# Performance work log

Measured on AMD Instinct MI355X. Metric: run time of the kernel, lower is better.

Reference implementation:

```python
import jax, jax.numpy as jnp
import numpy as np

STRIDE = 3


def _conv_block(x, W, b):
    # x: (B, L, C) -> windows (B, L-2, 3C) via fixed-stride slicing (faithful to scan_conv)
    B, L, C = x.shape
    Lw = L - STRIDE + 1
    win = jnp.concatenate([x[:, i:Lw + i, :] for i in range(STRIDE)], axis=-1)  # (B, Lw, 3C)
    y = jax.nn.leaky_relu(jnp.einsum('blk,ok->blo', win, W) + b)  # torch Linear: x @ W.T + b
    # zero_gate: zero rows of the *window* tensor zero the output
    mask = (jnp.sum(win, axis=2, keepdims=True) != 0).astype(y.dtype)
    y = y * mask
    # max_pool1d over sequence, kernel=2 stride=2 (floor)
    Lp = y.shape[1] // 2
    y = y[:, :2 * Lp, :].reshape(B, Lp, 2, -1).max(axis=2)
    return y


def setup_inputs() -> dict:
    key = jax.random.key(0)
    ks = jax.random.split(key, 16)
    B, PAD, E, IMG, V = 1024, 30, 512, 2048, 32000
    c1, c2, c3, lin2 = 200, 300, 300, 400
    lin1_in = 2 * c3 + IMG  # flattened (B,2,300) + image -> 600 + 2048
    s = 0.02
    return {
        'image_vectors': jax.random.normal(ks[0], (B, IMG), jnp.float32),
        'sentences': jax.random.randint(ks[1], (B, PAD), 0, V, jnp.int32),
        'embed_table': jax.random.normal(ks[2], (V, E), jnp.float32),
        'W1': jax.random.normal(ks[3], (c1, E * STRIDE), jnp.float32) * s,
        'b1': jnp.zeros((c1,), jnp.float32),
        'W2': jax.random.normal(ks[4], (c2, c1 * STRIDE), jnp.float32) * s,
        'b2': jnp.zeros((c2,), jnp.float32),
        'W3': jax.random.normal(ks[5], (c3, c2 * STRIDE), jnp.float32) * s,
        'b3': jnp.zeros((c3,), jnp.float32),
        'Wm': jax.random.normal(ks[6], (lin2, lin1_in), jnp.float32) * s,
        'bm': jnp.zeros((lin2,), jnp.float32),
        'Wo': jax.random.normal(ks[7], (1, lin2), jnp.float32) * s,
        'bo': jnp.zeros((1,), jnp.float32),
    }


def reference(image_vectors, sentences, embed_table, W1, b1, W2, b2, W3, b3, Wm, bm, Wo, bo):
    x = embed_table[sentences]                       # (B, 30, 512)
    x = _conv_block(x, W1, b1)                       # (B, 14, 200)
    x = _conv_block(x, W2, b2)                       # (B, 6, 300)
    x = _conv_block(x, W3, b3)                       # (B, 2, 300)
    B = x.shape[0]
    feats = jnp.concatenate([x.reshape(B, -1), image_vectors], axis=1)  # (B, 2648)
    h = jax.nn.leaky_relu(feats @ Wm.T + bm)         # (B, 400)
    out = h @ Wo.T + bo                              # (B, 1)
    return out
```

## Files before the change

kernel.cpp:

```cpp
#include <hip/hip_runtime.h>
#include <hip/hip_bf16.h>

#define LEAKY(v) ((v) > 0.0f ? (v) : 0.01f * (v))

constexpr int B_   = 1024;
constexpr int PAD  = 30;
constexpr int E    = 512;
constexpr int IMG  = 2048;
constexpr int C1   = 200;
constexpr int C2   = 300;
constexpr int C3   = 300;
constexpr int LIN2 = 400;

constexpr int NT1P = 16, KT1 = 48;
constexpr int NT2P = 20, KT2 = 21;
constexpr int NT3P = 24, KT3 = 30;
constexpr int NTMP = 28, KTM = 83;
constexpr int FK  = 2656;

constexpr int T1 = NT1P * KT1;
constexpr int T2 = NT2P * KT2;
constexpr int T3 = NT3P * KT3;
constexpr int TM = NTMP * KTM;
constexpr int TTOT = T1 + T2 + T3 + TM;

typedef __attribute__((ext_vector_type(8))) short bf16x8;
typedef __attribute__((ext_vector_type(4))) float f32x4;

__device__ inline unsigned short f2bf(float f) {
    __hip_bfloat16 h = __float2bfloat16(f);
    return *reinterpret_cast<unsigned short*>(&h);
}
__device__ inline float bf2f(unsigned short u) {
    unsigned int b = ((unsigned int)u) << 16;
    return __uint_as_float(b);
}

__global__ __launch_bounds__(256) void convert_all(
    const float* __restrict__ W1, const float* __restrict__ W2,
    const float* __restrict__ W3, const float* __restrict__ Wm,
    unsigned short* __restrict__ W1t, unsigned short* __restrict__ W2t,
    unsigned short* __restrict__ W3t, unsigned short* __restrict__ Wmt)
{
    int idx = blockIdx.x * 256 + threadIdx.x;
    if (idx >= TTOT * 64) return;
    int lane = idx & 63, t = idx >> 6;
    unsigned short v[8];

    if (t < T1) {
        int kk = t % KT1, nt = t / KT1;
        int ch = nt * 16 + (lane & 15);
        int k0 = kk * 32 + (lane >> 4) * 8;
        #pragma unroll
        for (int j = 0; j < 8; ++j)
            v[j] = (ch < C1) ? f2bf(W1[(size_t)ch * (3*E) + k0 + j]) : (unsigned short)0;
        ushort4* dst = reinterpret_cast<ushort4*>(W1t) + (size_t)t * 128 + lane * 2;
        dst[0] = ushort4{v[0],v[1],v[2],v[3]};
        dst[1] = ushort4{v[4],v[5],v[6],v[7]};
    } else if (t < T1 + T2) {
        int tt = t - T1;
        int kk = tt % KT2, nt = tt / KT2;
        int ch = nt * 16 + (lane & 15);
        int rowoff = kk / 7;
        int cbase  = (kk % 7) * 32 + (lane >> 4) * 8;
        #pragma unroll
        for (int j = 0; j < 8; ++j) {
            int c = cbase + j;
            v[j] = (ch < C2 && c < C1) ? f2bf(W2[(size_t)ch * (3*C1) + rowoff * C1 + c])
                                       : (unsigned short)0;
        }
        ushort4* dst = reinterpret_cast<ushort4*>(W2t) + (size_t)tt * 128 + lane * 2;
        dst[0] = ushort4{v[0],v[1],v[2],v[3]};
        dst[1] = ushort4{v[4],v[5],v[6],v[7]};
    } else if (t < T1 + T2 + T3) {
        int tt = t - T1 - T2;
        int kk = tt % KT3, nt = tt / KT3;
        int ch = nt * 16 + (lane & 15);
        int rowoff = kk / 10;
        int cbase  = (kk % 10) * 32 + (lane >> 4) * 8;
        #pragma unroll
        for (int j = 0; j < 8; ++j) {
            int c = cbase + j;
            v[j] = (ch < C3 && c < C2) ? f2bf(W3[(size_t)ch * (3*C2) + rowoff * C2 + c])
                                       : (unsigned short)0;
        }
        ushort4* dst = reinterpret_cast<ushort4*>(W3t) + (size_t)tt * 128 + lane * 2;
        dst[0] = ushort4{v[0],v[1],v[2],v[3]};
        dst[1] = ushort4{v[4],v[5],v[6],v[7]};
    } else {
        int tt = t - T1 - T2 - T3;
        int kk = tt % KTM, nt = tt / KTM;
        int ch = nt * 16 + (lane & 15);
        int kbase = kk * 32 + (lane >> 4) * 8;
        #pragma unroll
        for (int j = 0; j < 8; ++j) {
            int k = kbase + j;
            v[j] = (ch < LIN2 && k < 2648) ? f2bf(Wm[(size_t)ch * 2648 + k])
                                           : (unsigned short)0;
        }
        ushort4* dst = reinterpret_cast<ushort4*>(Wmt) + (size_t)tt * 128 + lane * 2;
        dst[0] = ushort4{v[0],v[1],v[2],v[3]};
        dst[1] = ushort4{v[4],v[5],v[6],v[7]};
    }
}

__global__ __launch_bounds__(512, 4) void conv_fused(
    const int* __restrict__ sent, const float* __restrict__ emb,
    const unsigned short* __restrict__ W1t, const float* __restrict__ b1,
    const unsigned short* __restrict__ W2t, const float* __restrict__ b2,
    const unsigned short* __restrict__ W3t, const float* __restrict__ b3,
    const float* __restrict__ image, unsigned short* __restrict__ feats)
{
    const int blk = blockIdx.x;
    const int tid = threadIdx.x;
    __shared__ unsigned short xs[66 * 512];
    __shared__ float rs[64];
    __shared__ float rs2[36];
    __shared__ float rs3[12];
    char* xsb = reinterpret_cast<char*>(xs);

    const int wid = tid >> 6, lane = tid & 63;
    const int kg = lane >> 4, trow = lane & 15, g = kg;

    for (int r = wid; r < 60; r += 8) {
        int bl = r / 30, rr = r % 30;
        int R = bl * 32 + rr;
        int row = sent[(2 * blk + bl) * PAD + rr];
        const float4* src = reinterpret_cast<const float4*>(emb + (size_t)row * E) + lane * 2;
        float4 e0 = src[0], e1 = src[1];
        float sum = e0.x + e0.y + e0.z + e0.w + e1.x + e1.y + e1.z + e1.w;
        union { ushort4 u4[2]; bf16x8 v; } pk;
        pk.u4[0] = ushort4{f2bf(e0.x), f2bf(e0.y), f2bf(e0.z), f2bf(e0.w)};
        pk.u4[1] = ushort4{f2bf(e1.x), f2bf(e1.y), f2bf(e1.z), f2bf(e1.w)};
        int byteoff = R * 1024 + ((lane ^ (R & 7)) << 4);
        *reinterpret_cast<bf16x8*>(xsb + byteoff) = pk.v;
        for (int off = 32; off; off >>= 1) sum += __shfl_down(sum, off);
        if (lane == 0) rs[R] = sum;
    }
    if (tid < 384) {
        int zi = tid >> 6;
        int R = (zi < 2) ? (30 + zi) : (60 + zi);
        int byteoff = R * 1024 + ((lane ^ (R & 7)) << 4);
        union { ushort4 u4[2]; bf16x8 v; } pk;
        pk.u4[0] = ushort4{0,0,0,0}; pk.u4[1] = ushort4{0,0,0,0};
        *reinterpret_cast<bf16x8*>(xsb + byteoff) = pk.v;
    }
    if (tid < 4) {
        const int pr[4] = {30, 31, 62, 63};
        rs[pr[tid]] = 0.f;
    }
    __syncthreads();

    const bf16x8* wb1 = reinterpret_cast<const bf16x8*>(W1t);
    const bf16x8* wp0 = wb1 + (size_t)((wid    ) * KT1) * 64 + lane;
    const bf16x8* wp1 = wb1 + (size_t)((wid + 8) * KT1) * 64 + lane;

    f32x4 c00={0,0,0,0},c01={0,0,0,0},c02={0,0,0,0},c03={0,0,0,0};
    f32x4 c10={0,0,0,0},c11={0,0,0,0},c12={0,0,0,0},c13={0,0,0,0};

    if (wid < 5) {
        #pragma unroll
        for (int rowoff = 0; rowoff < 3; ++rowoff) {
            const int R0 = trow + rowoff;
            const int R1 = R0 + 16, R2 = R0 + 32, R3 = R0 + 48;
            const int b3_0 = R0 * 1024 + (((R0 & 7) ^ kg) << 4);
            const int b3_1 = R1 * 1024 + (((R1 & 7) ^ kg) << 4);
            const int b3_2 = R2 * 1024 + (((R2 & 7) ^ kg) << 4);
            const int b3_3 = R3 * 1024 + (((R3 & 7) ^ kg) << 4);
            #pragma unroll
            for (int cc = 0; cc < 16; ++cc) {
                const int kk = rowoff * 16 + cc;
                bf16x8 a0 = *reinterpret_cast<const bf16x8*>(xsb + (b3_0 ^ (cc << 6)));
                bf16x8 a1 = *reinterpret_cast<const bf16x8*>(xsb + (b3_1 ^ (cc << 6)));
                bf16x8 a2 = *reinterpret_cast<const bf16x8*>(xsb + (b3_2 ^ (cc << 6)));
                bf16x8 a3 = *reinterpret_cast<const bf16x8*>(xsb + (b3_3 ^ (cc << 6)));
                bf16x8 b0 = wp0[kk * 64];
                bf16x8 b1v = wp1[kk * 64];
                c00 = __builtin_amdgcn_mfma_f32_16x16x32_bf16(a0, b0, c00, 0, 0, 0);
                c01 = __builtin_amdgcn_mfma_f32_16x16x32_bf16(a1, b0, c01, 0, 0, 0);
                c02 = __builtin_amdgcn_mfma_f32_16x16x32_bf16(a2, b0, c02, 0, 0, 0);
                c03 = __builtin_amdgcn_mfma_f32_16x16x32_bf16(a3, b0, c03, 0, 0, 0);
                c10 = __builtin_amdgcn_mfma_f32_16x16x32_bf16(a0, b1v, c10, 0, 0, 0);
                c11 = __builtin_amdgcn_mfma_f32_16x16x32_bf16(a1, b1v, c11, 0, 0, 0);
                c12 = __builtin_amdgcn_mfma_f32_16x16x32_bf16(a2, b1v, c12, 0, 0, 0);
                c13 = __builtin_amdgcn_mfma_f32_16x16x32_bf16(a3, b1v, c13, 0, 0, 0);
            }
        }
    } else {
        #pragma unroll
        for (int rowoff = 0; rowoff < 3; ++rowoff) {
            const int R0 = trow + rowoff;
            const int R1 = R0 + 16, R2 = R0 + 32, R3 = R0 + 48;
            const int b3_0 = R0 * 1024 + (((R0 & 7) ^ kg) << 4);
            const int b3_1 = R1 * 1024 + (((R1 & 7) ^ kg) << 4);
            const int b3_2 = R2 * 1024 + (((R2 & 7) ^ kg) << 4);
            const int b3_3 = R3 * 1024 + (((R3 & 7) ^ kg) << 4);
            #pragma unroll
            for (int cc = 0; cc < 16; ++cc) {
                const int kk = rowoff * 16 + cc;
                bf16x8 a0 = *reinterpret_cast<const bf16x8*>(xsb + (b3_0 ^ (cc << 6)));
                bf16x8 a1 = *reinterpret_cast<const bf16x8*>(xsb + (b3_1 ^ (cc << 6)));
                bf16x8 a2 = *reinterpret_cast<const bf16x8*>(xsb + (b3_2 ^ (cc << 6)));
                bf16x8 a3 = *reinterpret_cast<const bf16x8*>(xsb + (b3_3 ^ (cc << 6)));
                bf16x8 b0 = wp0[kk * 64];
                c00 = __builtin_amdgcn_mfma_f32_16x16x32_bf16(a0, b0, c00, 0, 0, 0);
                c01 = __builtin_amdgcn_mfma_f32_16x16x32_bf16(a1, b0, c01, 0, 0, 0);
                c02 = __builtin_amdgcn_mfma_f32_16x16x32_bf16(a2, b0, c02, 0, 0, 0);
                c03 = __builtin_amdgcn_mfma_f32_16x16x32_bf16(a3, b0, c03, 0, 0, 0);
            }
        }
    }
    __syncthreads();

    for (int idx = tid; idx < 36 * 32; idx += 512) {
        int r = idx >> 5, ck = idx & 31;
        union { ushort4 u4[2]; bf16x8 v; } pk;
        pk.u4[0] = ushort4{0,0,0,0}; pk.u4[1] = ushort4{0,0,0,0};
        *reinterpret_cast<bf16x8*>(xsb + r * 512 + (ck << 4)) = pk.v;
    }
    __syncthreads();

#define EPIM1(MT, CM) do {                                                       \
    int bl = (MT) >> 1;                                                          \
    int mloc = ((MT) & 1) * 16;                                                  \
    _Pragma("unroll")                                                            \
    for (int hf = 0; hf < 2; ++hf) {                                             \
        int wl = mloc + 4 * g + 2 * hf;                                          \
        int tp = wl >> 1;                                                        \
        if (tp < 14) {                                                           \
            float v0 = CM[2*hf] + bia, v1 = CM[2*hf+1] + bia;                    \
            v0 = LEAKY(v0); v1 = LEAKY(v1);                                      \
            int rb = bl * 32 + wl;                                               \
            if (rs[rb] + rs[rb+1] + rs[rb+2] == 0.f) v0 = 0.f;                   \
            if (rs[rb+1] + rs[rb+2] + rs[rb+3] == 0.f) v1 = 0.f;                 \
            int rg = bl * 18 + tp;                                               \
            int bo = rg * 512 + ((((ch) >> 3) ^ (rg & 7)) << 4) + ((ch) & 7) * 2;\
            *reinterpret_cast<unsigned short*>(xsb + bo) = f2bf(fmaxf(v0, v1));  \
        }                                                                        \
    }                                                                            \
} while (0)

#define EPI1(NTI, CA, CB, CC, CD) do {                                           \
    int ch = (wid + 8 * (NTI)) * 16 + trow;                                      \
    if (ch < C1) {                                                               \
        float bia = b1[ch];                                                      \
        EPIM1(0, CA); EPIM1(1, CB); EPIM1(2, CC); EPIM1(3, CD);                  \
    }                                                                            \
} while (0)

    EPI1(0, c00, c01, c02, c03);
    if (wid < 5) {
        EPI1(1, c10, c11, c12, c13);
    }
#undef EPI1
#undef EPIM1
    __syncthreads();

    for (int r = wid; r < 36; r += 8) {
        float s = 0.f;
        #pragma unroll
        for (int j = 0; j < 4; ++j) {
            int e = lane + 64 * j;
            int chunk = e >> 3, within = e & 7;
            s += bf2f(*reinterpret_cast<unsigned short*>(
                xsb + r * 512 + ((chunk ^ (r & 7)) << 4) + within * 2));
        }
        for (int off = 32; off; off >>= 1) s += __shfl_down(s, off);
        if (lane == 0) rs2[r] = s;
    }
    __syncthreads();

    const bf16x8* wb2 = reinterpret_cast<const bf16x8*>(W2t);
    const int nt2a = wid, nt2b = wid + 8;
    const int nt2c = (wid + 16 < NT2P) ? (wid + 16) : (NT2P - 1);
    const bf16x8* q0 = wb2 + (size_t)(nt2a * KT2) * 64 + lane;
    const bf16x8* q1 = wb2 + (size_t)(nt2b * KT2) * 64 + lane;
    const bf16x8* q2 = wb2 + (size_t)(nt2c * KT2) * 64 + lane;

    f32x4 d00={0,0,0,0},d01={0,0,0,0};
    f32x4 d10={0,0,0,0},d11={0,0,0,0};
    f32x4 d20={0,0,0,0},d21={0,0,0,0};

    {
        int kidx = 0;
        #pragma unroll
        for (int rowoff = 0; rowoff < 3; ++rowoff) {
            const int R0 = trow + rowoff;
            const int R1 = R0 + 18;
            const int b3_0 = R0 * 512 + (((R0 & 7) ^ kg) << 4);
            const int b3_1 = R1 * 512 + (((R1 & 7) ^ kg) << 4);
            #pragma unroll
            for (int cc = 0; cc < 7; ++cc, ++kidx) {
                bf16x8 a0 = *reinterpret_cast<const bf16x8*>(xsb + (b3_0 ^ (cc << 6)));
                bf16x8 a1 = *reinterpret_cast<const bf16x8*>(xsb + (b3_1 ^ (cc << 6)));
                bf16x8 b0 = q0[kidx * 64];
                bf16x8 b1v = q1[kidx * 64];
                bf16x8 b2v = q2[kidx * 64];
                d00 = __builtin_amdgcn_mfma_f32_16x16x32_bf16(a0, b0,  d00, 0, 0, 0);
                d01 = __builtin_amdgcn_mfma_f32_16x16x32_bf16(a1, b0,  d01, 0, 0, 0);
                d10 = __builtin_amdgcn_mfma_f32_16x16x32_bf16(a0, b1v, d10, 0, 0, 0);
                d11 = __builtin_amdgcn_mfma_f32_16x16x32_bf16(a1, b1v, d11, 0, 0, 0);
                d20 = __builtin_amdgcn_mfma_f32_16x16x32_bf16(a0, b2v, d20, 0, 0, 0);
                d21 = __builtin_amdgcn_mfma_f32_16x16x32_bf16(a1, b2v, d21, 0, 0, 0);
            }
        }
    }
    __syncthreads();

    for (int idx = tid; idx < 15 * 40; idx += 512) {
        int r = idx / 40, ck = idx % 40;
        union { ushort4 u4[2]; bf16x8 v; } pk;
        pk.u4[0] = ushort4{0,0,0,0}; pk.u4[1] = ushort4{0,0,0,0};
        *reinterpret_cast<bf16x8*>(xsb + r * 640 + (ck << 4)) = pk.v;
    }
    __syncthreads();

#define EPI2F(NT, DA, DB) do {                                                   \
    int ch = (NT) * 16 + trow;                                                   \
    if (ch < C2) {                                                               \
        float bia = b2[ch];                                                      \
        _Pragma("unroll")                                                        \
        for (int hf = 0; hf < 2; ++hf) {                                         \
            int t0 = 4 * g + 2 * hf;                                             \
            if (t0 < 12) {                                                       \
                { float v0 = LEAKY(DA[2*hf]   + bia);                            \
                  float v1 = LEAKY(DA[2*hf+1] + bia);                            \
                  if (rs2[t0] + rs2[t0+1] + rs2[t0+2] == 0.f) v0 = 0.f;          \
                  if (rs2[t0+1] + rs2[t0+2] + rs2[t0+3] == 0.f) v1 = 0.f;        \
                  int rg = (t0 >> 1);                                            \
                  int bo = rg * 640 + ((((ch)>>3) ^ (rg & 7)) << 4) + ((ch)&7)*2;\
                  *reinterpret_cast<unsigned short*>(xsb + bo) = f2bf(fmaxf(v0, v1)); } \
                { float v0 = LEAKY(DB[2*hf]   + bia);                            \
                  float v1 = LEAKY(DB[2*hf+1] + bia);                            \
                  int rb = 18 + t0;                                              \
                  if (rs2[rb] + rs2[rb+1] + rs2[rb+2] == 0.f) v0 = 0.f;          \
                  if (rs2[rb+1] + rs2[rb+2] + rs2[rb+3] == 0.f) v1 = 0.f;        \
                  int rg = 6 + (t0 >> 1);                                        \
                  int bo = rg * 640 + ((((ch)>>3) ^ (rg & 7)) << 4) + ((ch)&7)*2;\
                  *reinterpret_cast<unsigned short*>(xsb + bo) = f2bf(fmaxf(v0, v1)); } \
            }                                                                    \
        }                                                                        \
    }                                                                            \
} while (0)

    EPI2F(nt2a, d00, d01);
    EPI2F(nt2b, d10, d11);
    EPI2F(nt2c, d20, d21);
#undef EPI2F
    __syncthreads();

    for (int r = wid; r < 12; r += 8) {
        float s = 0.f;
        #pragma unroll
        for (int j = 0; j < 5; ++j) {
            int e = lane + 64 * j;
            int chunk = e >> 3, within = e & 7;
            s += bf2f(*reinterpret_cast<unsigned short*>(
                xsb + r * 640 + ((chunk ^ (r & 7)) << 4) + within * 2));
        }
        for (int off = 32; off; off >>= 1) s += __shfl_down(s, off);
        if (lane == 0) rs3[r] = s;
    }
    __syncthreads();

    const int rbase = (trow < 8) ? (6 * (trow >> 2) + (trow & 3)) : 12;

    const bf16x8* wb3 = reinterpret_cast<const bf16x8*>(W3t);
    const int nt3a = wid, nt3b = wid + 8;
    const int nt3c = (wid + 16 < NT3P) ? (wid + 16) : (NT3P - 1);
    const bf16x8* p0 = wb3 + (size_t)(nt3a * KT3) * 64 + lane;
    const bf16x8* p1 = wb3 + (size_t)(nt3b * KT3) * 64 + lane;
    const bf16x8* p2 = wb3 + (size_t)(nt3c * KT3) * 64 + lane;

    f32x4 e0={0,0,0,0},e1={0,0,0,0},e2={0,0,0,0};

    {
        int kidx = 0;
        #pragma unroll
        for (int rowoff = 0; rowoff < 3; ++rowoff) {
            const int R0 = rbase + rowoff;
            #pragma unroll
            for (int cc = 0; cc < 10; ++cc, ++kidx) {
                int chunk = cc * 4 + kg;
                bf16x8 a0 = *reinterpret_cast<const bf16x8*>(
                    xsb + R0 * 640 + ((chunk ^ (R0 & 7)) << 4));
                bf16x8 b0 = p0[kidx * 64];
                bf16x8 b1v = p1[kidx * 64];
                bf16x8 b2v = p2[kidx * 64];
                e0 = __builtin_amdgcn_mfma_f32_16x16x32_bf16(a0, b0,  e0, 0, 0, 0);
                e1 = __builtin_amdgcn_mfma_f32_16x16x32_bf16(a0, b1v, e1, 0, 0, 0);
                e2 = __builtin_amdgcn_mfma_f32_16x16x32_bf16(a0, b2v, e2, 0, 0, 0);
            }
        }
    }

#define EPI3F(NT, EM) do {                                                       \
    int ch = (NT) * 16 + trow;                                                   \
    if (ch < C3 && g < 2) {                                                      \
        float bia = b3[ch];                                                      \
        _Pragma("unroll")                                                        \
        for (int tp = 0; tp < 2; ++tp) {                                         \
            int rb = g * 6 + 2 * tp;                                             \
            float v0 = LEAKY(EM[2*tp]   + bia);                                  \
            float v1 = LEAKY(EM[2*tp+1] + bia);                                  \
            if (rs3[rb] + rs3[rb+1] + rs3[rb+2] == 0.f) v0 = 0.f;                \
            if (rs3[rb+1] + rs3[rb+2] + rs3[rb+3] == 0.f) v1 = 0.f;              \
            feats[(size_t)(2 * blk + g) * FK + tp * C3 + ch] = f2bf(fmaxf(v0, v1)); \
        }                                                                        \
    }                                                                            \
} while (0)

    EPI3F(nt3a, e0);
    EPI3F(nt3b, e1);
    EPI3F(nt3c, e2);
#undef EPI3F

    for (int idx = tid; idx < 2 * 257; idx += 512) {
        int bl = idx / 257, c = idx % 257;
        int b = 2 * blk + bl;
        if (c < 256) {
            const float4* src = reinterpret_cast<const float4*>(
                image + (size_t)b * IMG + c * 8);
            float4 a = src[0], d = src[1];
            ushort4* dst = reinterpret_cast<ushort4*>(feats + (size_t)b * FK + 600 + c * 8);
            dst[0] = ushort4{f2bf(a.x),f2bf(a.y),f2bf(a.z),f2bf(a.w)};
            dst[1] = ushort4{f2bf(d.x),f2bf(d.y),f2bf(d.z),f2bf(d.w)};
        } else {
            ushort4* dst = reinterpret_cast<ushort4*>(feats + (size_t)b * FK + 2648);
            dst[0] = ushort4{0,0,0,0};
            dst[1] = ushort4{0,0,0,0};
        }
    }
}

__global__ __launch_bounds__(256) void final_mfma(
    const unsigned short* __restrict__ feats, const unsigned short* __restrict__ Wmt,
    const float* __restrict__ bm, float* __restrict__ h)
{
    const int tid = threadIdx.x;
    const int wid = tid >> 6, lane = tid & 63;
    const int gw = blockIdx.x * 4 + wid;
    const int mt = gw / 14, q = gw % 14;
    const int kg = lane >> 4, trow = lane & 15, g = kg;
    const int m0 = mt * 16;

    const bf16x8* ap = reinterpret_cast<const bf16x8*>(feats)
                       + (size_t)(m0 + trow) * (FK / 8) + kg;
    const bf16x8* wb = reinterpret_cast<const bf16x8*>(Wmt);
    const bf16x8* wp0 = wb + (size_t)((q     ) * KTM) * 64 + lane;
    const bf16x8* wp1 = wb + (size_t)((q + 14) * KTM) * 64 + lane;

    f32x4 c0 = {0,0,0,0}, c1 = {0,0,0,0};

    bf16x8 aA = ap[0],     aB = ap[4];
    bf16x8 b0A = wp0[0],   b1A = wp1[0];
    bf16x8 b0B = wp0[64],  b1B = wp1[64];
    for (int kk = 0; kk < KTM - 2; ++kk) {
        bf16x8 a = aA, b0 = b0A, b1 = b1A;
        aA = aB; b0A = b0B; b1A = b1B;
        aB  = ap [(kk + 2) * 4];
        b0B = wp0[(kk + 2) * 64];
        b1B = wp1[(kk + 2) * 64];
        c0 = __builtin_amdgcn_mfma_f32_16x16x32_bf16(a, b0, c0, 0, 0, 0);
        c1 = __builtin_amdgcn_mfma_f32_16x16x32_bf16(a, b1, c1, 0, 0, 0);
    }
    c0 = __builtin_amdgcn_mfma_f32_16x16x32_bf16(aA, b0A, c0, 0, 0, 0);
    c1 = __builtin_amdgcn_mfma_f32_16x16x32_bf16(aA, b1A, c1, 0, 0, 0);
    c0 = __builtin_amdgcn_mfma_f32_16x16x32_bf16(aB, b0B, c0, 0, 0, 0);
    c1 = __builtin_amdgcn_mfma_f32_16x16x32_bf16(aB, b1B, c1, 0, 0, 0);

#define EPIM(NT, CM) do {                                                        \
    int ch = (NT) * 16 + trow;                                                   \
    if (ch < LIN2) {                                                             \
        float bia = bm[ch];                                                      \
        _Pragma("unroll")                                                        \
        for (int reg = 0; reg < 4; ++reg) {                                      \
            float v = LEAKY(CM[reg] + bia);                                      \
            h[(size_t)(m0 + 4 * g + reg) * LIN2 + ch] = v;                       \
        }                                                                        \
    }                                                                            \
} while (0)

    EPIM(q,      c0);
    EPIM(q + 14, c1);
#undef EPIM
}

__global__ __launch_bounds__(256) void final_reduce(
    const float* __restrict__ h, const float* __restrict__ Wo,
    const float* __restrict__ bo, float* __restrict__ out)
{
    const int tid = threadIdx.x;
    const int wid = tid >> 6, lane = tid & 63;
    const int b = blockIdx.x * 4 + wid;
    float s = 0.f;
    #pragma unroll
    for (int j = 0; j < 7; ++j) {
        int o = lane + 64 * j;
        if (o < LIN2) s += h[(size_t)b * LIN2 + o] * Wo[o];
    }
    for (int off = 32; off; off >>= 1) s += __shfl_down(s, off);
    if (lane == 0) out[b] = s + bo[0];
}

extern "C" void kernel_launch(void* const* d_in, const int* in_sizes, int n_in,
                              void* d_out, int out_size, void* d_ws, size_t ws_size,
                              hipStream_t stream) {
    const float* image = (const float*)d_in[0];
    const int*   sent  = (const int*)  d_in[1];
    const float* emb   = (const float*)d_in[2];
    const float* W1    = (const float*)d_in[3];
    const float* b1    = (const float*)d_in[4];
    const float* W2    = (const float*)d_in[5];
    const float* b2    = (const float*)d_in[6];
    const float* W3    = (const float*)d_in[7];
    const float* b3    = (const float*)d_in[8];
    const float* Wm    = (const float*)d_in[9];
    const float* bm    = (const float*)d_in[10];
    const float* Wo    = (const float*)d_in[11];
    const float* bo    = (const float*)d_in[12];
    float* out = (float*)d_out;

    unsigned short* W1t = (unsigned short*)d_ws;
    unsigned short* W2t = W1t + (size_t)T1 * 512;
    unsigned short* W3t = W2t + (size_t)T2 * 512;
    unsigned short* Wmt = W3t + (size_t)T3 * 512;
    unsigned short* feats = Wmt + (size_t)TM * 512;
    float* h = (float*)(feats + (size_t)B_ * FK);

    convert_all<<<(TTOT * 64 + 255) / 256, 256, 0, stream>>>(
        W1, W2, W3, Wm, W1t, W2t, W3t, Wmt);

    conv_fused<<<B_ / 2, 512, 0, stream>>>(
        sent, emb, W1t, b1, W2t, b2, W3t, b3, image, feats);

    final_mfma<<<224, 256, 0, stream>>>(feats, Wmt, bm, h);
    final_reduce<<<B_ / 4, 256, 0, stream>>>(h, Wo, bo, out);
}
```

Measured before the change: 99.65 us.

## Split layer-1 embedding staging into two K halves to halve shared memory

The embedding tile for the first conv is staged and consumed in two 256-column halves instead of one 512-column pass. This halves the static LDS buffer, which lets more workgroups fit on each CU. The cost is an extra staging round and barrier, a per-half row-sum accumulation, and a new swizzle on a 512-byte row pitch. It also clamps the third layer-3 weight tile for waves 3 and up to tile 19, which appears to avoid fetching padded tiles.

Result: no change. 98.41 us (median of 2 runs) (-1.3%).

```diff
diff --git a/kernel.cpp b/kernel.cpp
--- a/kernel.cpp
+++ b/kernel.cpp
@@ -113,7 +113,7 @@
 {
     const int blk = blockIdx.x;
     const int tid = threadIdx.x;
-    __shared__ unsigned short xs[66 * 512];
+    __shared__ unsigned short xs[66 * 256];
     __shared__ float rs[64];
     __shared__ float rs2[36];
     __shared__ float rs3[12];
@@ -122,35 +122,6 @@
     const int wid = tid >> 6, lane = tid & 63;
     const int kg = lane >> 4, trow = lane & 15, g = kg;
 
-    for (int r = wid; r < 60; r += 8) {
-        int bl = r / 30, rr = r % 30;
-        int R = bl * 32 + rr;
-        int row = sent[(2 * blk + bl) * PAD + rr];
-        const float4* src = reinterpret_cast<const float4*>(emb + (size_t)row * E) + lane * 2;
-        float4 e0 = src[0], e1 = src[1];
-        float sum = e0.x + e0.y + e0.z + e0.w + e1.x + e1.y + e1.z + e1.w;
-        union { ushort4 u4[2]; bf16x8 v; } pk;
-        pk.u4[0] = ushort4{f2bf(e0.x), f2bf(e0.y), f2bf(e0.z), f2bf(e0.w)};
-        pk.u4[1] = ushort4{f2bf(e1.x), f2bf(e1.y), f2bf(e1.z), f2bf(e1.w)};
-        int byteoff = R * 1024 + ((lane ^ (R & 7)) << 4);
-        *reinterpret_cast<bf16x8*>(xsb + byteoff) = pk.v;
-        for (int off = 32; off; off >>= 1) sum += __shfl_down(sum, off);
-        if (lane == 0) rs[R] = sum;
-    }
-    if (tid < 384) {
-        int zi = tid >> 6;
-        int R = (zi < 2) ? (30 + zi) : (60 + zi);
-        int byteoff = R * 1024 + ((lane ^ (R & 7)) << 4);
-        union { ushort4 u4[2]; bf16x8 v; } pk;
-        pk.u4[0] = ushort4{0,0,0,0}; pk.u4[1] = ushort4{0,0,0,0};
-        *reinterpret_cast<bf16x8*>(xsb + byteoff) = pk.v;
-    }
-    if (tid < 4) {
-        const int pr[4] = {30, 31, 62, 63};
-        rs[pr[tid]] = 0.f;
-    }
-    __syncthreads();
-
     const bf16x8* wb1 = reinterpret_cast<const bf16x8*>(W1t);
     const bf16x8* wp0 = wb1 + (size_t)((wid    ) * KT1) * 64 + lane;
     const bf16x8* wp1 = wb1 + (size_t)((wid + 8) * KT1) * 64 + lane;
@@ -158,55 +129,93 @@
     f32x4 c00={0,0,0,0},c01={0,0,0,0},c02={0,0,0,0},c03={0,0,0,0};
     f32x4 c10={0,0,0,0},c11={0,0,0,0},c12={0,0,0,0},c13={0,0,0,0};
 
-    if (wid < 5) {
-        #pragma unroll
-        for (int rowoff = 0; rowoff < 3; ++rowoff) {
-            const int R0 = trow + rowoff;
-            const int R1 = R0 + 16, R2 = R0 + 32, R3 = R0 + 48;
-            const int b3_0 = R0 * 1024 + (((R0 & 7) ^ kg) << 4);
-            const int b3_1 = R1 * 1024 + (((R1 & 7) ^ kg) << 4);
-            const int b3_2 = R2 * 1024 + (((R2 & 7) ^ kg) << 4);
-            const int b3_3 = R3 * 1024 + (((R3 & 7) ^ kg) << 4);
+    #pragma unroll
+    for (int h = 0; h < 2; ++h) {
+        if (h == 1) __syncthreads();
+
+        #pragma unroll
+        for (int r8 = 0; r8 < 8; ++r8) {
+            int r = wid + 8 * r8;
+            if (r < 60) {
+                int bl = r / 30, rr = r % 30;
+                int R = bl * 32 + rr;
+                int row = sent[(2 * blk + bl) * PAD + rr];
+                float4 e = reinterpret_cast<const float4*>(
+                    emb + (size_t)row * E + h * 256)[lane];
+                float sum = e.x + e.y + e.z + e.w;
+                ushort4 pk4{f2bf(e.x), f2bf(e.y), f2bf(e.z), f2bf(e.w)};
+                int c = lane >> 1;
+                int bo = R * 512 + ((c ^ (R & 7)) << 4) + (lane & 1) * 8;
+                *reinterpret_cast<ushort4*>(xsb + bo) = pk4;
+                for (int off = 32; off; off >>= 1) sum += __shfl_down(sum, off);
+                if (lane == 0) { if (h == 0) rs[R] = sum; else rs[R] += sum; }
+            }
+        }
+        if (tid < 384) {
+            int zi = tid >> 6;
+            int R = (zi < 2) ? (30 + zi) : (60 + zi);
+            int c = lane >> 1;
+            int bo = R * 512 + ((c ^ (R & 7)) << 4) + (lane & 1) * 8;
+            *reinterpret_cast<ushort4*>(xsb + bo) = ushort4{0,0,0,0};
+        }
+        if (h == 0 && tid < 4) {
+            const int pr[4] = {30, 31, 62, 63};
+            rs[pr[tid]] = 0.f;
+        }
+        __syncthreads();
+
+        if (wid < 5) {
             #pragma unroll
-            for (int cc = 0; cc < 16; ++cc) {
-                const int kk = rowoff * 16 + cc;
-                bf16x8 a0 = *reinterpret_cast<const bf16x8*>(xsb + (b3_0 ^ (cc << 6)));
-                bf16x8 a1 = *reinterpret_cast<const bf16x8*>(xsb + (b3_1 ^ (cc << 6)));
-                bf16x8 a2 = *reinterpret_cast<const bf16x8*>(xsb + (b3_2 ^ (cc << 6)));
-                bf16x8 a3 = *reinterpret_cast<const bf16x8*>(xsb + (b3_3 ^ (cc << 6)));
-                bf16x8 b0 = wp0[kk * 64];
-                bf16x8 b1v = wp1[kk * 64];
-                c00 = __builtin_amdgcn_mfma_f32_16x16x32_bf16(a0, b0, c00, 0, 0, 0);
-                c01 = __builtin_amdgcn_mfma_f32_16x16x32_bf16(a1, b0, c01, 0, 0, 0);
-                c02 = __builtin_amdgcn_mfma_f32_16x16x32_bf16(a2, b0, c02, 0, 0, 0);
-                c03 = __builtin_amdgcn_mfma_f32_16x16x32_bf16(a3, b0, c03, 0, 0, 0);
-                c10 = __builtin_amdgcn_mfma_f32_16x16x32_bf16(a0, b1v, c10, 0, 0, 0);
-                c11 = __builtin_amdgcn_mfma_f32_16x16x32_bf16(a1, b1v, c11, 0, 0, 0);
-                c12 = __builtin_amdgcn_mfma_f32_16x16x32_bf16(a2, b1v, c12, 0, 0, 0);
-                c13 = __builtin_amdgcn_mfma_f32_16x16x32_bf16(a3, b1v, c13, 0, 0, 0);
+            for (int rowoff = 0; rowoff < 3; ++rowoff) {
+                const int R0 = trow + rowoff;
+                const int R1 = R0 + 16, R2 = R0 + 32, R3 = R0 + 48;
+                #pragma unroll
+                for (int cc = 0; cc < 8; ++cc) {
+                    const int kk = rowoff * 16 + h * 8 + cc;
+                    const int ch2 = cc * 4 + kg;
+                    bf16x8 a0 = *reinterpret_cast<const bf16x8*>(
+                        xsb + R0 * 512 + (((ch2) ^ (R0 & 7)) << 4));
+                    bf16x8 a1 = *reinterpret_cast<const bf16x8*>(
+                        xsb + R1 * 512 + (((ch2) ^ (R1 & 7)) << 4));
+                    bf16x8 a2 = *reinterpret_cast<const bf16x8*>(
+                        xsb + R2 * 512 + (((ch2) ^ (R2 & 7)) << 4));
+                    bf16x8 a3 = *reinterpret_cast<const bf16x8*>(
+                        xsb + R3 * 512 + (((ch2) ^ (R3 & 7)) << 4));
+                    bf16x8 b0 = wp0[kk * 64];
+                    bf16x8 b1v = wp1[kk * 64];
+                    c00 = __builtin_amdgcn_mfma_f32_16x16x32_bf16(a0, b0, c00, 0, 0, 0);
+                    c01 = __builtin_amdgcn_mfma_f32_16x16x32_bf16(a1, b0, c01, 0, 0, 0);
+                    c02 = __builtin_amdgcn_mfma_f32_16x16x32_bf16(a2, b0, c02, 0, 0, 0);
+                    c03 = __builtin_amdgcn_mfma_f32_16x16x32_bf16(a3, b0, c03, 0, 0, 0);
+                    c10 = __builtin_amdgcn_mfma_f32_16x16x32_bf16(a0, b1v, c10, 0, 0, 0);
+                    c11 = __builtin_amdgcn_mfma_f32_16x16x32_bf16(a1, b1v, c11, 0, 0, 0);
+                    c12 = __builtin_amdgcn_mfma_f32_16x16x32_bf16(a2, b1v, c12, 0, 0, 0);
+                    c13 = __builtin_amdgcn_mfma_f32_16x16x32_bf16(a3, b1v, c13, 0, 0, 0);
+                }
             }
-        }
-    } else {
-        #pragma unroll
-        for (int rowoff = 0; rowoff < 3; ++rowoff) {
-            const int R0 = trow + rowoff;
-            const int R1 = R0 + 16, R2 = R0 + 32, R3 = R0 + 48;
-            const int b3_0 = R0 * 1024 + (((R0 & 7) ^ kg) << 4);
-            const int b3_1 = R1 * 1024 + (((R1 & 7) ^ kg) << 4);
-            const int b3_2 = R2 * 1024 + (((R2 & 7) ^ kg) << 4);
-            const int b3_3 = R3 * 1024 + (((R3 & 7) ^ kg) << 4);
+        } else {
             #pragma unroll
-            for (int cc = 0; cc < 16; ++cc) {
-                const int kk = rowoff * 16 + cc;
-                bf16x8 a0 = *reinterpret_cast<const bf16x8*>(xsb + (b3_0 ^ (cc << 6)));
-                bf16x8 a1 = *reinterpret_cast<const bf16x8*>(xsb + (b3_1 ^ (cc << 6)));
-                bf16x8 a2 = *reinterpret_cast<const bf16x8*>(xsb + (b3_2 ^ (cc << 6)));
-                bf16x8 a3 = *reinterpret_cast<const bf16x8*>(xsb + (b3_3 ^ (cc << 6)));
-                bf16x8 b0 = wp0[kk * 64];
-                c00 = __builtin_amdgcn_mfma_f32_16x16x32_bf16(a0, b0, c00, 0, 0, 0);
-                c01 = __builtin_amdgcn_mfma_f32_16x16x32_bf16(a1, b0, c01, 0, 0, 0);
-                c02 = __builtin_amdgcn_mfma_f32_16x16x32_bf16(a2, b0, c02, 0, 0, 0);
-                c03 = __builtin_amdgcn_mfma_f32_16x16x32_bf16(a3, b0, c03, 0, 0, 0);
+            for (int rowoff = 0; rowoff < 3; ++rowoff) {
+                const int R0 = trow + rowoff;
+                const int R1 = R0 + 16, R2 = R0 + 32, R3 = R0 + 48;
+                #pragma unroll
+                for (int cc = 0; cc < 8; ++cc) {
+                    const int kk = rowoff * 16 + h * 8 + cc;
+                    const int ch2 = cc * 4 + kg;
+                    bf16x8 a0 = *reinterpret_cast<const bf16x8*>(
+                        xsb + R0 * 512 + (((ch2) ^ (R0 & 7)) << 4));
+                    bf16x8 a1 = *reinterpret_cast<const bf16x8*>(
+                        xsb + R1 * 512 + (((ch2) ^ (R1 & 7)) << 4));
+                    bf16x8 a2 = *reinterpret_cast<const bf16x8*>(
+                        xsb + R2 * 512 + (((ch2) ^ (R2 & 7)) << 4));
+                    bf16x8 a3 = *reinterpret_cast<const bf16x8*>(
+                        xsb + R3 * 512 + (((ch2) ^ (R3 & 7)) << 4));
+                    bf16x8 b0 = wp0[kk * 64];
+                    c00 = __builtin_amdgcn_mfma_f32_16x16x32_bf16(a0, b0, c00, 0, 0, 0);
+                    c01 = __builtin_amdgcn_mfma_f32_16x16x32_bf16(a1, b0, c01, 0, 0, 0);
+                    c02 = __builtin_amdgcn_mfma_f32_16x16x32_bf16(a2, b0, c02, 0, 0, 0);
+                    c03 = __builtin_amdgcn_mfma_f32_16x16x32_bf16(a3, b0, c03, 0, 0, 0);
+                }
             }
         }
     }
@@ -367,7 +376,7 @@
 
     const bf16x8* wb3 = reinterpret_cast<const bf16x8*>(W3t);
     const int nt3a = wid, nt3b = wid + 8;
-    const int nt3c = (wid + 16 < NT3P) ? (wid + 16) : (NT3P - 1);
+    const int nt3c = (wid < 3) ? (wid + 16) : 19;
     const bf16x8* p0 = wb3 + (size_t)(nt3a * KT3) * 64 + lane;
     const bf16x8* p1 = wb3 + (size_t)(nt3b * KT3) * 64 + lane;
     const bf16x8* p2 = wb3 + (size_t)(nt3c * KT3) * 64 + lane;
```
